# Optimization experiments

Measured on AMD Instinct MI355X. Metric: run time of the kernel, lower is better.

The kernel has to match this reference:

```python
import jax, jax.numpy as jnp
import numpy as np

KH, KW, STRIDE, PAD = 3, 3, 1, 1


def unfold(img, kh, kw, stride, padding):
    # torch.nn.functional.unfold, transposed to [B, L, C*kh*kw] with (c, kh, kw)-major ordering
    b, c, h, w = img.shape
    p = jnp.pad(img, ((0, 0), (0, 0), (padding, padding), (padding, padding)))
    oh = (h - kh + 2 * padding) // stride + 1
    ow = (w - kw + 2 * padding) // stride + 1
    # [b, c, kh*kw, oh, ow]; static python loop over the 9 kernel offsets only
    cols = jnp.stack([p[:, :, i:i + oh * stride:stride, j:j + ow * stride:stride]
                      for i in range(kh) for j in range(kw)], axis=2)
    return cols.reshape(b, c * kh * kw, oh * ow).transpose(0, 2, 1), oh, ow


def setup_inputs() -> dict:
    key = jax.random.key(0)
    k1, k2 = jax.random.split(key)
    img = jax.random.normal(k1, (8, 64, 112, 112), dtype=jnp.float32)
    weights = 0.8 * jax.random.normal(k2, (64, 64, 3, 3), dtype=jnp.float32)
    return {"img": img, "weights": weights}


def reference(img, weights):
    b = img.shape[0]
    O = weights.shape[0]
    W = weights.reshape(O, -1)            # [O, K], K = in_ch*kh*kw
    K = W.shape[1]
    u, oh, ow = unfold(img, KH, KW, STRIDE, PAD)   # [b, L, K]
    u2 = u * u
    u3 = u2 * u

    def gemm(poly):
        return jnp.einsum('blk,ok->blo', poly, W)

    # f: identity-kernel term has all-zero coefficients (p00=p10=p20=p30=0) -> drops out
    f = gemm(-0.000287 + 0.266 * u - 0.1097 * u2) / 75

    # identity_kernel is all ones, so (const*ones) @ ones.T == const * K (scalar)
    g1 = (0.11 / 75) * K + gemm(0.001309 + 0.00619 * u - 0.009 * u2 + 0.001383 * u3)
    g2 = (0.179 / 75) * K + gemm(-0.0025 + 0.00303 * u - 0.00484 * u2 + 0.0175 * u3)
    g3 = (0.238 / 75) * K + gemm(-0.000954 + 0.00187 * u + 0.001877 * u2 + 0.01502 * u3)
    g4 = (0.388 / 75) * K + gemm(-0.00734 + 0.001117 * u + 0.00752 * u2 + 0.009 * u3)
    g5 = (0.507 / 75) * K + gemm(-0.01017 + 0.000426 * u + 0.00837 * u2 + 0.00413 * u3)

    sig = jax.nn.sigmoid
    s1 = sig(10 * (0.15 - f))
    s2 = sig(10 * (f - 0.15)) + sig(10 * (0.23 - f)) - 1
    s3 = sig(10 * (f - 0.23)) + sig(10 * (0.32 - f)) - 1
    s4 = sig(10 * (f - 0.32)) + sig(10 * (0.39 - f)) - 1
    s5 = sig(10 * (f - 0.39))

    out = s1 * g1 + s2 * g2 + s3 * g3 + s4 * g4 + s5 * g5   # [b, L, O]
    return out.transpose(0, 2, 1).reshape(b, O, oh, ow)
```

## Files before the change

### kernel.cpp

```cpp
#include <hip/hip_runtime.h>

#define HW   112
#define KK   576

typedef __attribute__((ext_vector_type(8))) short s16x8;
typedef __attribute__((ext_vector_type(4))) float f32x4;
typedef __attribute__((ext_vector_type(2))) float f32x2;

#define LP_ROW   1184
#define LP_PHASE (10 * LP_ROW)
#define SWZ(px)  (((px) & 3) ^ (((px) >> 2) & 3))

__device__ inline unsigned short f2bf(float f) {
    unsigned u = __float_as_uint(f);
    u += 0x7FFF + ((u >> 16) & 1);
    return (unsigned short)(u >> 16);
}
__device__ inline unsigned pack2(float lo, float hi) {
    return (unsigned)f2bf(lo) | ((unsigned)f2bf(hi) << 16);
}

__global__ __launch_bounds__(256) void prep_w(const float* __restrict__ W,
                                              unsigned short* __restrict__ wb,
                                              float* __restrict__ S) {
    const int bid = blockIdx.x, t = threadIdx.x;
    if (bid < 144) {
        const int i   = bid * 256 + t;
        const int j   = i & 7;
        const int l   = (i >> 3) & 63;
        const int nt  = (i >> 9) & 3;
        const int cc  = (i >> 11) & 1;
        const int tap = i >> 12;
        const int c   = cc * 32 + ((l >> 4) << 3) + j;
        const int o   = nt * 16 + (l & 15);
        wb[i] = f2bf(W[o * KK + c * 9 + tap]);
    } else {
        __shared__ float partial[256];
        const int o = t >> 2, part = t & 3;
        const float4* row = (const float4*)(W + o * KK) + part * 36;
        float s = 0.f;
        for (int k = 0; k < 36; ++k) { float4 v = row[k]; s += v.x + v.y + v.z + v.w; }
        partial[t] = s;
        __syncthreads();
        if (part == 0) S[o] = partial[t] + partial[t + 1] + partial[t + 2] + partial[t + 3];
    }
}

__global__ __launch_bounds__(256, 3) void conv_fused(const float* __restrict__ img,
                                                     const unsigned short* __restrict__ wb,
                                                     const float* __restrict__ S,
                                                     float* __restrict__ out) {
    __shared__ __align__(16) char tile[3 * LP_PHASE];

    const int t = threadIdx.x, wv = t >> 6, lane = t & 63;
    const int m = lane & 15, q = lane >> 4;

    const int bid = blockIdx.x;
    const int b = bid & 7;
    const int rest = bid >> 3;
    const int oc2 = rest & 1;
    const int r = rest >> 1;
    const int ty = r / 7, tx = r - ty * 7;
    const int y0 = ty * 8, x0 = tx * 16;

    f32x4 acc[3][2][2];
    #pragma unroll
    for (int p = 0; p < 3; ++p)
        #pragma unroll
        for (int at = 0; at < 2; ++at)
            #pragma unroll
            for (int ntl = 0; ntl < 2; ++ntl)
                acc[p][at][ntl] = (f32x4){0.f, 0.f, 0.f, 0.f};

    const char* wbase = (const char*)wb + oc2 * 2048 + lane * 16;
    s16x8 bfr[9][2];

    #pragma unroll 1
    for (int cc = 0; cc < 2; ++cc) {
        if (cc) __syncthreads();

        if (t < 160) {
            const int cp = t & 15, row = t >> 4;
            const int y = y0 + row - 1;
            float va[2][18];
            if (y < 0 || y >= HW) {
                #pragma unroll
                for (int e = 0; e < 2; ++e)
                    #pragma unroll
                    for (int px = 0; px < 18; ++px) va[e][px] = 0.f;
            } else {
                #pragma unroll
                for (int e = 0; e < 2; ++e) {
                    const float* rp = img + ((size_t)(b * 64 + cc * 32 + cp * 2 + e) * HW + y) * HW;
                    va[e][0] = (x0 > 0) ? rp[x0 - 1] : 0.f;
                    #pragma unroll
                    for (int i2 = 0; i2 < 4; ++i2) {
                        const float4 v = *(const float4*)(rp + x0 + i2 * 4);
                        va[e][1 + 4 * i2] = v.x;
                        va[e][2 + 4 * i2] = v.y;
                        va[e][3 + 4 * i2] = v.z;
                        va[e][4 + 4 * i2] = v.w;
                    }
                    va[e][17] = (x0 + 16 < HW) ? rp[x0 + 16] : 0.f;
                }
            }
            char* wp = tile + row * LP_ROW + (cp & 3) * 4;
            #pragma unroll
            for (int px = 0; px < 18; ++px) {
                char* a0 = wp + px * 64 + (((cp >> 2) ^ SWZ(px)) << 4);
                const float l1 = va[0][px], h1 = va[1][px];
                const float l2 = l1 * l1,   h2 = h1 * h1;
                const float l3 = l2 * l1,   h3 = h2 * h1;
                *(unsigned*)(a0)                = pack2(l1, h1);
                *(unsigned*)(a0 + LP_PHASE)     = pack2(l2, h2);
                *(unsigned*)(a0 + 2 * LP_PHASE) = pack2(l3, h3);
            }
        }

        #pragma unroll
        for (int tap = 0; tap < 9; ++tap)
            #pragma unroll
            for (int ntl = 0; ntl < 2; ++ntl)
                bfr[tap][ntl] = *(const s16x8*)(wbase + (tap * 2 + cc) * 4096 + ntl * 1024);

        __syncthreads();

        #pragma unroll
        for (int p = 0; p < 3; ++p) {
            const char* base = tile + p * LP_PHASE;
            #pragma unroll
            for (int kx = 0; kx < 3; ++kx) {
                const int pxr  = m + kx;
                const int c8sr = q ^ SWZ(pxr);
                const int abase = wv * (2 * LP_ROW) + pxr * 64 + c8sr * 16;
                s16x8 af[4];
                #pragma unroll
                for (int r4 = 0; r4 < 4; ++r4)
                    af[r4] = *(const s16x8*)&base[abase + r4 * LP_ROW];
                __builtin_amdgcn_s_setprio(1);
                #pragma unroll
                for (int ky = 0; ky < 3; ++ky)
                    #pragma unroll
                    for (int at = 0; at < 2; ++at)
                        #pragma unroll
                        for (int ntl = 0; ntl < 2; ++ntl)
                            acc[p][at][ntl] = __builtin_amdgcn_mfma_f32_16x16x32_bf16(
                                af[at + ky], bfr[ky * 3 + kx][ntl], acc[p][at][ntl], 0, 0, 0);
                __builtin_amdgcn_s_setprio(0);
            }
        }
    }

    #pragma unroll
    for (int ntl = 0; ntl < 2; ++ntl) {
        const int o = (oc2 * 2 + ntl) * 16 + (lane & 15);
        const float Sv = S[o];
        const float fS = -0.000287f / 75.f * Sv;
        const float cg1 = 0.8448f  + 0.001309f * Sv;
        const float D1  = 0.52992f - 0.003809f * Sv;
        const float D2  = 0.45312f + 0.001546f * Sv;
        const float D3  = 1.152f   - 0.006386f * Sv;
        const float D4  = 0.91392f - 0.00283f  * Sv;
        #pragma unroll
        for (int at = 0; at < 2; ++at) {
            float res[4];
            #pragma unroll
            for (int h = 0; h < 2; ++h) {
                const f32x2 u1 = {acc[0][at][ntl][2 * h], acc[0][at][ntl][2 * h + 1]};
                const f32x2 u2 = {acc[1][at][ntl][2 * h], acc[1][at][ntl][2 * h + 1]};
                const f32x2 u3 = {acc[2][at][ntl][2 * h], acc[2][at][ntl][2 * h + 1]};
                const f32x2 f  = fS   + 0.00354667f * u1 - 0.00146267f * u2;
                const f32x2 g1 = cg1  + 0.00619f    * u1 - 0.009f      * u2 + 0.001383f * u3;
                const f32x2 d1 = D1   - 0.00316f    * u1 + 0.00416f    * u2 + 0.016117f * u3;
                const f32x2 d2 = D2   - 0.00116f    * u1 + 0.006717f   * u2 - 0.00248f  * u3;
                const f32x2 d3 = D3   - 0.000753f   * u1 + 0.005643f   * u2 - 0.00602f  * u3;
                const f32x2 d4 = D4   - 0.000691f   * u1 + 0.00085f    * u2 - 0.00487f  * u3;
                f32x2 E;
                E.x = __expf(-10.f * f.x);
                E.y = __expf(-10.f * f.y);
                const f32x2 den1 = 1.f + E * 4.4816890703f;
                const f32x2 den2 = 1.f + E * 9.9741824548f;
                const f32x2 den3 = 1.f + E * 24.5325301971f;
                const f32x2 den4 = 1.f + E * 49.4024491055f;
                f32x2 o2 = g1;
                o2.x += __builtin_amdgcn_rcpf(den1.x) * d1.x + __builtin_amdgcn_rcpf(den2.x) * d2.x
                      + __builtin_amdgcn_rcpf(den3.x) * d3.x + __builtin_amdgcn_rcpf(den4.x) * d4.x;
                o2.y += __builtin_amdgcn_rcpf(den1.y) * d1.y + __builtin_amdgcn_rcpf(den2.y) * d2.y
                      + __builtin_amdgcn_rcpf(den3.y) * d3.y + __builtin_amdgcn_rcpf(den4.y) * d4.y;
                res[2 * h] = o2.x; res[2 * h + 1] = o2.y;
            }
            const int y = y0 + 2 * wv + at;
            float* op = out + (((size_t)(b * 64 + o)) * HW + y) * HW + x0 + q * 4;
            *(float4*)op = make_float4(res[0], res[1], res[2], res[3]);
        }
    }
}

extern "C" void kernel_launch(void* const* d_in, const int* in_sizes, int n_in,
                              void* d_out, int out_size, void* d_ws, size_t ws_size,
                              hipStream_t stream) {
    const float* img = (const float*)d_in[0];
    const float* w   = (const float*)d_in[1];
    float* outp = (float*)d_out;
    unsigned short* wb = (unsigned short*)d_ws;
    float* S = (float*)(wb + 36864);

    hipLaunchKernelGGL(prep_w,     dim3(145),  dim3(256), 0, stream, w, wb, S);
    hipLaunchKernelGGL(conv_fused, dim3(1568), dim3(256), 0, stream, img, wb, S, outp);
}
```

Before: 109.8 us.

## Double-buffer LDS tile to overlap second channel-half load with MFMA compute

Splits the shared tile into two buffers so the global load, cube and pack of the second 32-channel half overlaps the first plane's MFMAs, removing one barrier-separated serial phase. It also swaps the manual round-to-nearest bf16 conversion for the hardware v_cvt_pk_bf16_f32 packed instruction. Shared memory doubles and the occupancy hint drops from 3 to 2 blocks per CU, which reduces latency hiding across blocks.

New measurement: 110.3 us. About the same (+0.5%).

```diff
diff --git a/kernel.cpp b/kernel.cpp
--- a/kernel.cpp
+++ b/kernel.cpp
@@ -17,7 +17,9 @@
     return (unsigned short)(u >> 16);
 }
 __device__ inline unsigned pack2(float lo, float hi) {
-    return (unsigned)f2bf(lo) | ((unsigned)f2bf(hi) << 16);
+    unsigned r;
+    asm("v_cvt_pk_bf16_f32 %0, %1, %2" : "=v"(r) : "v"(lo), "v"(hi));
+    return r;
 }
 
 __global__ __launch_bounds__(256) void prep_w(const float* __restrict__ W,
@@ -46,11 +48,11 @@
     }
 }
 
-__global__ __launch_bounds__(256, 3) void conv_fused(const float* __restrict__ img,
+__global__ __launch_bounds__(256, 2) void conv_fused(const float* __restrict__ img,
                                                      const unsigned short* __restrict__ wb,
                                                      const float* __restrict__ S,
                                                      float* __restrict__ out) {
-    __shared__ __align__(16) char tile[3 * LP_PHASE];
+    __shared__ __align__(16) char tile[2][3 * LP_PHASE];
 
     const int t = threadIdx.x, wv = t >> 6, lane = t & 63;
     const int m = lane & 15, q = lane >> 4;
@@ -75,81 +77,103 @@
     const char* wbase = (const char*)wb + oc2 * 2048 + lane * 16;
     s16x8 bfr[9][2];
 
-    #pragma unroll 1
-    for (int cc = 0; cc < 2; ++cc) {
-        if (cc) __syncthreads();
-
-        if (t < 160) {
-            const int cp = t & 15, row = t >> 4;
-            const int y = y0 + row - 1;
-            float va[2][18];
-            if (y < 0 || y >= HW) {
-                #pragma unroll
-                for (int e = 0; e < 2; ++e)
-                    #pragma unroll
-                    for (int px = 0; px < 18; ++px) va[e][px] = 0.f;
-            } else {
-                #pragma unroll
-                for (int e = 0; e < 2; ++e) {
-                    const float* rp = img + ((size_t)(b * 64 + cc * 32 + cp * 2 + e) * HW + y) * HW;
-                    va[e][0] = (x0 > 0) ? rp[x0 - 1] : 0.f;
-                    #pragma unroll
-                    for (int i2 = 0; i2 < 4; ++i2) {
-                        const float4 v = *(const float4*)(rp + x0 + i2 * 4);
-                        va[e][1 + 4 * i2] = v.x;
-                        va[e][2 + 4 * i2] = v.y;
-                        va[e][3 + 4 * i2] = v.z;
-                        va[e][4 + 4 * i2] = v.w;
-                    }
-                    va[e][17] = (x0 + 16 < HW) ? rp[x0 + 16] : 0.f;
-                }
-            }
-            char* wp = tile + row * LP_ROW + (cp & 3) * 4;
-            #pragma unroll
-            for (int px = 0; px < 18; ++px) {
-                char* a0 = wp + px * 64 + (((cp >> 2) ^ SWZ(px)) << 4);
-                const float l1 = va[0][px], h1 = va[1][px];
-                const float l2 = l1 * l1,   h2 = h1 * h1;
-                const float l3 = l2 * l1,   h3 = h2 * h1;
-                *(unsigned*)(a0)                = pack2(l1, h1);
-                *(unsigned*)(a0 + LP_PHASE)     = pack2(l2, h2);
-                *(unsigned*)(a0 + 2 * LP_PHASE) = pack2(l3, h3);
-            }
-        }
-
+    const int cp = t & 15, srow = t >> 4;
+    const int sy = y0 + srow - 1;
+
+    auto loadW = [&](int cc) {
         #pragma unroll
         for (int tap = 0; tap < 9; ++tap)
             #pragma unroll
             for (int ntl = 0; ntl < 2; ++ntl)
                 bfr[tap][ntl] = *(const s16x8*)(wbase + (tap * 2 + cc) * 4096 + ntl * 1024);
-
-        __syncthreads();
-
-        #pragma unroll
-        for (int p = 0; p < 3; ++p) {
-            const char* base = tile + p * LP_PHASE;
-            #pragma unroll
-            for (int kx = 0; kx < 3; ++kx) {
-                const int pxr  = m + kx;
-                const int c8sr = q ^ SWZ(pxr);
-                const int abase = wv * (2 * LP_ROW) + pxr * 64 + c8sr * 16;
-                s16x8 af[4];
+    };
+
+    auto load_va = [&](int cc, float (&va)[2][18]) {
+        if (t >= 160) return;
+        if (sy < 0 || sy >= HW) {
+            #pragma unroll
+            for (int e = 0; e < 2; ++e)
                 #pragma unroll
-                for (int r4 = 0; r4 < 4; ++r4)
-                    af[r4] = *(const s16x8*)&base[abase + r4 * LP_ROW];
-                __builtin_amdgcn_s_setprio(1);
+                for (int px = 0; px < 18; ++px) va[e][px] = 0.f;
+        } else {
+            #pragma unroll
+            for (int e = 0; e < 2; ++e) {
+                const float* rp = img + ((size_t)(b * 64 + cc * 32 + cp * 2 + e) * HW + sy) * HW;
+                va[e][0] = (x0 > 0) ? rp[x0 - 1] : 0.f;
                 #pragma unroll
-                for (int ky = 0; ky < 3; ++ky)
+                for (int i2 = 0; i2 < 4; ++i2) {
+                    const float4 v = *(const float4*)(rp + x0 + i2 * 4);
+                    va[e][1 + 4 * i2] = v.x;
+                    va[e][2 + 4 * i2] = v.y;
+                    va[e][3 + 4 * i2] = v.z;
+                    va[e][4 + 4 * i2] = v.w;
+                }
+                va[e][17] = (x0 + 16 < HW) ? rp[x0 + 16] : 0.f;
+            }
+        }
+    };
+
+    auto pack_write = [&](const float (&va)[2][18], char* buf) {
+        if (t >= 160) return;
+        char* wp = buf + srow * LP_ROW + (cp & 3) * 4;
+        #pragma unroll
+        for (int px = 0; px < 18; ++px) {
+            char* a0 = wp + px * 64 + (((cp >> 2) ^ SWZ(px)) << 4);
+            const float l1 = va[0][px], h1 = va[1][px];
+            const float l2 = l1 * l1,   h2 = h1 * h1;
+            const float l3 = l2 * l1,   h3 = h2 * h1;
+            *(unsigned*)(a0)                = pack2(l1, h1);
+            *(unsigned*)(a0 + LP_PHASE)     = pack2(l2, h2);
+            *(unsigned*)(a0 + 2 * LP_PHASE) = pack2(l3, h3);
+        }
+    };
+
+    auto compute_plane = [&](const char* bufbase, int p) {
+        const char* base = bufbase + p * LP_PHASE;
+        #pragma unroll
+        for (int kx = 0; kx < 3; ++kx) {
+            const int pxr  = m + kx;
+            const int c8sr = q ^ SWZ(pxr);
+            const int abase = wv * (2 * LP_ROW) + pxr * 64 + c8sr * 16;
+            s16x8 af[4];
+            #pragma unroll
+            for (int r4 = 0; r4 < 4; ++r4)
+                af[r4] = *(const s16x8*)&base[abase + r4 * LP_ROW];
+            __builtin_amdgcn_s_setprio(1);
+            #pragma unroll
+            for (int ky = 0; ky < 3; ++ky)
+                #pragma unroll
+                for (int at = 0; at < 2; ++at)
                     #pragma unroll
-                    for (int at = 0; at < 2; ++at)
-                        #pragma unroll
-                        for (int ntl = 0; ntl < 2; ++ntl)
-                            acc[p][at][ntl] = __builtin_amdgcn_mfma_f32_16x16x32_bf16(
-                                af[at + ky], bfr[ky * 3 + kx][ntl], acc[p][at][ntl], 0, 0, 0);
-                __builtin_amdgcn_s_setprio(0);
-            }
-        }
-    }
+                    for (int ntl = 0; ntl < 2; ++ntl)
+                        acc[p][at][ntl] = __builtin_amdgcn_mfma_f32_16x16x32_bf16(
+                            af[at + ky], bfr[ky * 3 + kx][ntl], acc[p][at][ntl], 0, 0, 0);
+            __builtin_amdgcn_s_setprio(0);
+        }
+    };
+
+    {
+        float va[2][18];
+        load_va(0, va);
+        pack_write(va, tile[0]);
+    }
+    loadW(0);
+    __syncthreads();
+
+    {
+        float vb[2][18];
+        load_va(1, vb);
+        compute_plane(tile[0], 0);
+        pack_write(vb, tile[1]);
+    }
+    compute_plane(tile[0], 1);
+    compute_plane(tile[0], 2);
+    loadW(1);
+    __syncthreads();
+
+    compute_plane(tile[1], 0);
+    compute_plane(tile[1], 1);
+    compute_plane(tile[1], 2);
 
     #pragma unroll
     for (int ntl = 0; ntl < 2; ++ntl) {
```
